# Kernel optimization log

Hardware: AMD Instinct MI355X
Metric: run time of the kernel (lower is better)

## Reference

```python
import jax, jax.numpy as jnp
import numpy as np

NUM_HEADS = 16
HEAD_DIM = 80  # head_dim_ori; NPU pads 80->128 with zeros (math-neutral)


def _rotate_half(x):
    x1, x2 = jnp.split(x, 2, axis=-1)
    return jnp.concatenate([-x2, x1], axis=-1)


def setup_inputs() -> dict:
    key = jax.random.key(0)
    ks = jax.random.split(key, 7)
    S, E = 4096, 1280
    inv = jnp.asarray(1.0 / np.sqrt(E), jnp.float32)
    # rotary tables: proper cos/sin from angles for realism
    pos = jnp.arange(S, dtype=jnp.float32)[:, None]
    freqs = 1.0 / (10000.0 ** (jnp.arange(0, HEAD_DIM // 2, dtype=jnp.float32) / (HEAD_DIM // 2)))
    ang = pos * freqs[None, :]                      # [S, 40]
    ang = jnp.concatenate([ang, ang], axis=-1)      # [S, 80] rotate-half layout
    return {
        'hidden_states': jax.random.normal(ks[0], (S, E), jnp.float32),
        'cos': jnp.cos(ang),
        'sin': jnp.sin(ang),
        'w_qkv': jax.random.normal(ks[1], (3 * E, E), jnp.float32) * inv,
        'b_qkv': jax.random.normal(ks[2], (3 * E,), jnp.float32) * 0.02,
        'w_proj': jax.random.normal(ks[3], (E, E), jnp.float32) * inv,
        'b_proj': jax.random.normal(ks[4], (E,), jnp.float32) * 0.02,
    }


def reference(hidden_states, cos, sin, w_qkv, b_qkv, w_proj, b_proj):
    S, E = hidden_states.shape
    H, D = NUM_HEADS, HEAD_DIM
    # fused QKV linear (transposeB=True, hasBias=True) then split into 3
    qkv = hidden_states @ w_qkv.T + b_qkv          # [S, 3E]
    q, k, v = jnp.split(qkv, 3, axis=-1)
    q = q.reshape(S, H, D)
    k = k.reshape(S, H, D)
    v = v.reshape(S, H, D)
    # rotate-half RoPE (rotaryCoeff=2) on q and k
    c = cos[:, None, :]
    s = sin[:, None, :]
    q = q * c + _rotate_half(q) * s
    k = k * c + _rotate_half(k) * s
    # full bidirectional self-attention (PA_ENCODER), qkScale = 1/sqrt(head_dim_ori)
    scale = jnp.asarray(1.0 / np.sqrt(D), q.dtype)
    scores = jnp.einsum('shd,thd->hst', q, k) * scale   # [H, S, S]
    attn = jax.nn.softmax(scores, axis=-1)
    out = jnp.einsum('hst,thd->shd', attn, v).reshape(S, E)
    # output projection + residual add (atten_res_add)
    dense = out @ w_proj.T + b_proj
    return hidden_states + dense
```

## Files before the change

kernel.cpp:

```cpp
#include <hip/hip_runtime.h>
#include <hip/hip_bf16.h>


#define S_LEN 4096
#define E_DIM 1280
#define NH 16
#define HD 80
#define HDP 96

typedef __bf16 bf16x8 __attribute__((ext_vector_type(8)));
typedef float f32x4 __attribute__((ext_vector_type(4)));

__device__ __forceinline__ short f2bf(float x) {
    __hip_bfloat16 h = __float2bfloat16(x);
    return __builtin_bit_cast(short, h);
}
__device__ __forceinline__ float bf2f(short x) {
    return __bfloat162float(__builtin_bit_cast(__hip_bfloat16, x));
}
__device__ __forceinline__ bf16x8 ldb(const short* p) {
    return *reinterpret_cast<const bf16x8*>(p);
}
__device__ __forceinline__ unsigned cvt_pk_bf16(float a, float b) {
    unsigned r;
    asm("v_cvt_pk_bf16_f32 %0, %1, %2" : "=v"(r) : "v"(a), "v"(b));
    return r;
}
__device__ __forceinline__ void gload16(const void* g, void* l) {
    __builtin_amdgcn_global_load_lds(
        (const __attribute__((address_space(1))) unsigned int*)g,
        (__attribute__((address_space(3))) unsigned int*)l, 16, 0, 0);
}

__global__ __launch_bounds__(256) void cast3_k(const float* __restrict__ a, short* __restrict__ oa, int na4,
                                               const float* __restrict__ b, short* __restrict__ ob, int nb4,
                                               const float* __restrict__ c, short* __restrict__ oc, int nc4,
                                               short* __restrict__ Qg, short* __restrict__ Kg, int nd4) {
    int j = blockIdx.x * 256 + threadIdx.x;
    const float* src;
    short* dst;
    bool remap = false;
    if (j < na4) {
        src = a; dst = oa;
    } else {
        j -= na4;
        if (j < nb4) {
            src = b; dst = ob; remap = true;
        } else {
            j -= nb4;
            if (j < nc4) {
                src = c; dst = oc;
            } else {
                j -= nc4;
                if (j >= nd4) return;
                int half = nd4 >> 1;
                short* base = (j < half) ? Qg : Kg;
                int rem = (j < half) ? j : j - half;
                int hs = rem >> 1, gp = rem & 1;
                int4 z = {0, 0, 0, 0};
                *reinterpret_cast<int4*>(&base[(size_t)hs * HDP + 80 + gp * 8]) = z;
                return;
            }
        }
    }
    float4 v = *reinterpret_cast<const float4*>(&src[j * 4]);
    int dj = j;
    if (remap) {
        int row = j / 320, c4 = j - row * 320;
        if (row < 2560) {
            int part = row / 1280;
            int loc = row - part * 1280;
            int hh = loc / 80, d = loc - hh * 80;
            int dp = (d < 40) ? 2 * d : 2 * (d - 40) + 1;
            dj = (part * 1280 + hh * 80 + dp) * 320 + c4;
        }
    }
    ushort4 o;
    o.x = (unsigned short)f2bf(v.x);
    o.y = (unsigned short)f2bf(v.y);
    o.z = (unsigned short)f2bf(v.z);
    o.w = (unsigned short)f2bf(v.w);
    *reinterpret_cast<ushort4*>(&dst[dj * 4]) = o;
}

__global__ __launch_bounds__(512, 2) void gemm1_256_k(
    const short* __restrict__ A, const short* __restrict__ B, const float* __restrict__ bias,
    const float* __restrict__ cosp, const float* __restrict__ sinp,
    short* __restrict__ Qg, short* __restrict__ Kg, short* __restrict__ Vt) {
    const int K = E_DIM;
    __shared__ __align__(16) short smem[65536];
#define AS_(d, kh) (smem + (d)*16384 + (kh)*8192)
#define BS_(d, kh) (smem + 32768 + (d)*16384 + (kh)*8192)
    int t = threadIdx.x;
    int lane = t & 63, w = t >> 6;
    int wr = w >> 2, wc = w & 3;
    int lr = lane & 15, lg = lane >> 4;
    int bid = blockIdx.x;
    int swz = (bid & 7) * 30 + (bid >> 3);
    int bm = swz / 15, bn = swz % 15;
    int mb = bm * 256, nb = bn * 256;

    int lgs = (t & 3) ^ ((t >> 3) & 3);
    const short* aS = A + (size_t)(mb + (t >> 2)) * K + lgs * 8;
    const short* bS = B + (size_t)(nb + (t >> 2)) * K + lgs * 8;
    const int rowStep = 128 * K;

    int aoff[2][4], boff[4];
#pragma unroll
    for (int mq = 0; mq < 2; mq++)
#pragma unroll
        for (int ii = 0; ii < 4; ii++) {
            int r = wr * 128 + mq * 64 + ii * 16 + lr;
            aoff[mq][ii] = r * 32 + ((lg ^ ((r >> 1) & 3)) * 8);
        }
#pragma unroll
    for (int n = 0; n < 4; n++) {
        int r = wc * 64 + n * 16 + lr;
        boff[n] = r * 32 + ((lg ^ ((r >> 1) & 3)) * 8);
    }

    f32x4 acc[8][4];
#pragma unroll
    for (int i = 0; i < 8; i++)
#pragma unroll
        for (int n = 0; n < 4; n++) acc[i][n] = (f32x4){0.f, 0.f, 0.f, 0.f};

#define STG_A(d, kh, kb2)                                              \
    {                                                                  \
        gload16(aS + (kb2) + (kh)*32, AS_(d, kh) + w * 512);           \
        gload16(aS + rowStep + (kb2) + (kh)*32, AS_(d, kh) + 4096 + w * 512); \
    }
#define STG_B(d, kh, kb2)                                              \
    {                                                                  \
        gload16(bS + (kb2) + (kh)*32, BS_(d, kh) + w * 512);           \
        gload16(bS + rowStep + (kb2) + (kh)*32, BS_(d, kh) + 4096 + w * 512); \
    }

    STG_A(0, 0, 0);
    STG_B(0, 0, 0);
    STG_A(0, 1, 0);
    STG_B(0, 1, 0);
    asm volatile("s_waitcnt vmcnt(4)" ::: "memory");
    __builtin_amdgcn_s_barrier();
    asm volatile("" ::: "memory");

    for (int kb = 0; kb < K; kb += 64) {
        int d = (kb >> 6) & 1;
        int kb2 = kb + 64;
        bool more = kb2 < K;
        bf16x8 af[4], bfr[4];

#pragma unroll
        for (int n = 0; n < 4; n++) bfr[n] = ldb(&BS_(d, 0)[boff[n]]);
#pragma unroll
        for (int ii = 0; ii < 4; ii++) af[ii] = ldb(&AS_(d, 0)[aoff[0][ii]]);
        if (more) STG_A(d ^ 1, 0, kb2);
        __builtin_amdgcn_s_barrier();
        asm volatile("s_waitcnt lgkmcnt(0)" ::: "memory");
        __builtin_amdgcn_sched_barrier(0);
        __builtin_amdgcn_s_setprio(1);
#pragma unroll
        for (int ii = 0; ii < 4; ii++)
#pragma unroll
            for (int n = 0; n < 4; n++)
                acc[ii][n] = __builtin_amdgcn_mfma_f32_16x16x32_bf16(af[ii], bfr[n], acc[ii][n], 0, 0, 0);
        __builtin_amdgcn_s_setprio(0);
        __builtin_amdgcn_s_barrier();
        asm volatile("" ::: "memory");

#pragma unroll
        for (int ii = 0; ii < 4; ii++) af[ii] = ldb(&AS_(d, 0)[aoff[1][ii]]);
        if (more) {
            STG_B(d ^ 1, 0, kb2);
            asm volatile("s_waitcnt vmcnt(4)" ::: "memory");
        } else {
            asm volatile("s_waitcnt vmcnt(0)" ::: "memory");
        }
        __builtin_amdgcn_s_barrier();
        asm volatile("s_waitcnt lgkmcnt(0)" ::: "memory");
        __builtin_amdgcn_sched_barrier(0);
        __builtin_amdgcn_s_setprio(1);
#pragma unroll
        for (int ii = 0; ii < 4; ii++)
#pragma unroll
            for (int n = 0; n < 4; n++)
                acc[4 + ii][n] = __builtin_amdgcn_mfma_f32_16x16x32_bf16(af[ii], bfr[n], acc[4 + ii][n], 0, 0, 0);
        __builtin_amdgcn_s_setprio(0);
        __builtin_amdgcn_s_barrier();
        asm volatile("" ::: "memory");

#pragma unroll
        for (int n = 0; n < 4; n++) bfr[n] = ldb(&BS_(d, 1)[boff[n]]);
#pragma unroll
        for (int ii = 0; ii < 4; ii++) af[ii] = ldb(&AS_(d, 1)[aoff[0][ii]]);
        if (more) STG_A(d ^ 1, 1, kb2);
        __builtin_amdgcn_s_barrier();
        asm volatile("s_waitcnt lgkmcnt(0)" ::: "memory");
        __builtin_amdgcn_sched_barrier(0);
        __builtin_amdgcn_s_setprio(1);
#pragma unroll
        for (int ii = 0; ii < 4; ii++)
#pragma unroll
            for (int n = 0; n < 4; n++)
                acc[ii][n] = __builtin_amdgcn_mfma_f32_16x16x32_bf16(af[ii], bfr[n], acc[ii][n], 0, 0, 0);
        __builtin_amdgcn_s_setprio(0);
        __builtin_amdgcn_s_barrier();
        asm volatile("" ::: "memory");

#pragma unroll
        for (int ii = 0; ii < 4; ii++) af[ii] = ldb(&AS_(d, 1)[aoff[1][ii]]);
        if (more) {
            STG_B(d ^ 1, 1, kb2);
            asm volatile("s_waitcnt vmcnt(4)" ::: "memory");
        }
        __builtin_amdgcn_s_barrier();
        asm volatile("s_waitcnt lgkmcnt(0)" ::: "memory");
        __builtin_amdgcn_sched_barrier(0);
        __builtin_amdgcn_s_setprio(1);
#pragma unroll
        for (int ii = 0; ii < 4; ii++)
#pragma unroll
            for (int n = 0; n < 4; n++)
                acc[4 + ii][n] = __builtin_amdgcn_mfma_f32_16x16x32_bf16(af[ii], bfr[n], acc[4 + ii][n], 0, 0, 0);
        __builtin_amdgcn_s_setprio(0);
        __builtin_amdgcn_s_barrier();
        asm volatile("" ::: "memory");
    }
#undef STG_A
#undef STG_B

    int part = nb / E_DIM;
    int nloc = nb - part * E_DIM;
    if (part < 2) {
#pragma unroll
        for (int j = 0; j < 4; j++) {
            int c = wc * 64 + j * 16 + lr;
            int pcol = nloc + c;
            int hh = pcol / 80, dl = pcol - hh * 80;
            float bv = bias[part * E_DIM + hh * 80 + ((dl & 1) ? (dl >> 1) + 40 : (dl >> 1))];
            int cw = c & 7, cg = c >> 3;
#pragma unroll
            for (int i = 0; i < 8; i++) {
#pragma unroll
                for (int r = 0; r < 4; r++) {
                    int s = wr * 128 + (i >> 2) * 64 + (i & 3) * 16 + lg * 4 + r;
                    smem[s * 256 + (((cg ^ ((s >> 2) & 3)) << 3) | cw)] = f2bf(acc[i][j][r] + bv);
                }
            }
        }
        __syncthreads();
        short* dst = part ? Kg : Qg;
        const float qs = part ? 1.0f : 0.16129849190f;
#pragma unroll
        for (int k = 0; k < 16; k++) {
            int g = t + k * 512;
            int row = g >> 5, gc = g & 31;
            int pg = gc ^ ((row >> 2) & 3);
            int4 v = *reinterpret_cast<const int4*>(&smem[row * 256 + pg * 8]);
            int s = mb + row;
            int pcol = nloc + gc * 8;
            int hh = pcol / 80;
            int dl = pcol - hh * 80;
            int i2 = dl >> 1;
            float4 cs = *reinterpret_cast<const float4*>(&cosp[s * HD + i2]);
            float4 sn = *reinterpret_cast<const float4*>(&sinp[s * HD + i2]);
            const short* sp = reinterpret_cast<const short*>(&v);
            float f[8];
#pragma unroll
            for (int i = 0; i < 8; i++) f[i] = bf2f(sp[i]);
            float c0 = cs.x * qs, s0 = sn.x * qs;
            float c1 = cs.y * qs, s1 = sn.y * qs;
            float c2 = cs.z * qs, s2 = sn.z * qs;
            float c3 = cs.w * qs, s3 = sn.w * qs;
            uint4 pw;
            pw.x = cvt_pk_bf16(f[0] * c0 - f[1] * s0, f[1] * c0 + f[0] * s0);
            pw.y = cvt_pk_bf16(f[2] * c1 - f[3] * s1, f[3] * c1 + f[2] * s1);
            pw.z = cvt_pk_bf16(f[4] * c2 - f[5] * s2, f[5] * c2 + f[4] * s2);
            pw.w = cvt_pk_bf16(f[6] * c3 - f[7] * s3, f[7] * c3 + f[6] * s3);
            *reinterpret_cast<uint4*>(&dst[((size_t)hh * S_LEN + s) * HDP + dl]) = pw;
        }
    } else {
#pragma unroll
        for (int j = 0; j < 4; j++) {
            int c = wc * 64 + j * 16 + lr;
            float bv = bias[nb + c];
            int cw = c & 7, cg = c >> 3;
#pragma unroll
            for (int i = 0; i < 8; i++) {
#pragma unroll
                for (int r = 0; r < 4; r++) {
                    int s = wr * 128 + (i >> 2) * 64 + (i & 3) * 16 + lg * 4 + r;
                    int vs = ((s >> 2) & 7) ^ ((s >> 5) & 7);
                    smem[s * 256 + (((cg ^ vs) << 3) | cw)] = f2bf(acc[i][j][r] + bv);
                }
            }
        }
        __syncthreads();
#pragma unroll
        for (int k = 0; k < 16; k++) {
            int g = t + k * 512;
            int lc = g >> 5;
            int sgrp = (g >> 2) & 7, oct = g & 3;
            int cg = lc >> 3, cw = lc & 7;
            short tmp[8];
#pragma unroll
            for (int q = 0; q < 8; q++) {
                int key = oct * 4 + (q & 3) + ((q >> 2) << 4);
                int sl = sgrp * 32 + key;
                int vs = (key >> 2) ^ sgrp;
                tmp[q] = smem[sl * 256 + (((cg ^ vs) << 3) | cw)];
            }
            int vcol = nloc + lc;
            int hh = vcol / 80, dl = vcol - hh * 80;
            *reinterpret_cast<int4*>(
                &Vt[(size_t)(hh * HD + dl) * S_LEN + mb + sgrp * 32 + oct * 8]) =
                *reinterpret_cast<int4*>(tmp);
        }
    }
#undef AS_
#undef BS_
}

__global__ __launch_bounds__(256) void gemm_bt_k(
    const short* __restrict__ A, const short* __restrict__ B, const float* __restrict__ bias,
    const float* __restrict__ resid, float* __restrict__ Out) {
    const int K = E_DIM;
    __shared__ short As[2][128 * 64];
    __shared__ short Bs[2][128 * 64];
    int t = threadIdx.x;
    int lane = t & 63, w = t >> 6;
    int wr = w >> 1, wc = w & 1;
    int lr = lane & 15, lg = lane >> 4;
    int mb = blockIdx.y * 128, nb = blockIdx.x * 128;

    const short* asrc[4];
    const short* bsrc[4];
#pragma unroll
    for (int c = 0; c < 4; c++) {
        int p = c * 256 + t;
        int m = p >> 3;
        int kg = (p & 7) ^ (m & 7);
        asrc[c] = A + (size_t)(mb + m) * K + kg * 8;
        bsrc[c] = B + (size_t)(nb + m) * K + kg * 8;
    }
    int xa = lr & 7;
    int cx0 = ((0 * 4 + lg) ^ xa) * 8;
    int cx1 = ((1 * 4 + lg) ^ xa) * 8;
    int rowA[4], rowB[4];
#pragma unroll
    for (int i = 0; i < 4; i++) {
        rowA[i] = (wr * 64 + i * 16 + lr) * 64;
        rowB[i] = (wc * 64 + i * 16 + lr) * 64;
    }

    f32x4 acc[4][4];
#pragma unroll
    for (int i = 0; i < 4; i++)
#pragma unroll
        for (int j = 0; j < 4; j++) acc[i][j] = (f32x4){0.f, 0.f, 0.f, 0.f};

#define G_STAGE(buf, kb)                                             \
    {                                                                \
        _Pragma("unroll") for (int c = 0; c < 4; c++) {              \
            int ldso = c * 2048 + w * 512;                           \
            gload16(asrc[c] + (kb), &As[buf][ldso]);                 \
            gload16(bsrc[c] + (kb), &Bs[buf][ldso]);                 \
        }                                                            \
    }

    G_STAGE(0, 0);
    asm volatile("s_waitcnt vmcnt(0)" ::: "memory");
    __syncthreads();

    int buf = 0;
    for (int kb = 0; kb < K; kb += 64) {
        if (kb + 64 < K) G_STAGE(buf ^ 1, kb + 64);
        __builtin_amdgcn_s_setprio(1);
#pragma unroll
        for (int kk = 0; kk < 2; kk++) {
            int cx = kk ? cx1 : cx0;
            bf16x8 af[4], bfr[4];
#pragma unroll
            for (int i = 0; i < 4; i++) {
                af[i] = ldb(&As[buf][rowA[i] + cx]);
                bfr[i] = ldb(&Bs[buf][rowB[i] + cx]);
            }
#pragma unroll
            for (int i = 0; i < 4; i++)
#pragma unroll
                for (int j = 0; j < 4; j++)
                    acc[i][j] = __builtin_amdgcn_mfma_f32_16x16x32_bf16(af[i], bfr[j], acc[i][j], 0, 0, 0);
        }
        __builtin_amdgcn_s_setprio(0);
        __syncthreads();
        buf ^= 1;
    }
#undef G_STAGE

#pragma unroll
    for (int j = 0; j < 4; j++) {
        int n = nb + wc * 64 + j * 16 + lr;
        float bv = bias[n];
#pragma unroll
        for (int i = 0; i < 4; i++) {
#pragma unroll
            for (int r = 0; r < 4; r++) {
                int s = mb + wr * 64 + i * 16 + lg * 4 + r;
                Out[s * E_DIM + n] = acc[i][j][r] + bv + resid[s * E_DIM + n];
            }
        }
    }
}

__global__ __launch_bounds__(512, 4) void attn_k(const short* __restrict__ Qg,
                                                 const short* __restrict__ Kg,
                                                 const short* __restrict__ Vt,
                                                 short* __restrict__ Ob) {
    __shared__ __align__(16) short smem[24832];
    short* ksb = smem;
    short* vsb = smem + 13312;

    int t = threadIdx.x;
    int lane = t & 63, w = t >> 6;
    int lr = lane & 15, lg = lane >> 4;
    int pairi = w >> 1, half = w & 1;
    int L = blockIdx.x;
    int h = ((L & 7) << 1) | (L >> 8);
    int qb = ((L >> 3) & 31) << 7;

    const short* kgp = Kg + (size_t)h * S_LEN * HDP;
    const short* vgp = Vt + (size_t)h * HD * S_LEN;

    bf16x8 qf[2][3];
#pragma unroll
    for (int qq = 0; qq < 2; qq++) {
        const short* qp = Qg + ((size_t)h * S_LEN + qb + pairi * 32 + qq * 16 + lr) * HDP;
#pragma unroll
        for (int kk = 0; kk < 3; kk++) qf[qq][kk] = ldb(qp + kk * 32 + lg * 8);
    }
    f32x4 o[2][5];
#pragma unroll
    for (int qq = 0; qq < 2; qq++)
#pragma unroll
        for (int nd = 0; nd < 5; nd++) o[qq][nd] = (f32x4){0.f, 0.f, 0.f, 0.f};
    f32x4 l4[2] = {(f32x4){0.f, 0.f, 0.f, 0.f}, (f32x4){0.f, 0.f, 0.f, 0.f}};

    int gk0 = t, rk0 = gk0 / 13, ok0 = gk0 % 13;
    if (ok0 == 12) ok0 = 0;
    const short* ksrc0 = kgp + rk0 * HDP + ok0 * 8;
    int gk1 = t + 512, rk1 = gk1 / 13, ok1 = gk1 % 13;
    if (ok1 == 12) ok1 = 0;
    const short* ksrc1 = kgp + rk1 * HDP + ok1 * 8;
    int gv0 = t, rv0 = gv0 / 9, ov0 = gv0 % 9;
    if (ov0 == 8) ov0 = 0;
    const short* vsrc0 = vgp + (size_t)rv0 * S_LEN + ov0 * 8;
    bool v1v = (t + 512) < 720;
    int gv1 = t + 512, rv1 = gv1 / 9, ov1 = gv1 % 9;
    if (ov1 == 8) ov1 = 0;
    const short* vsrc1 = vgp + (size_t)rv1 * S_LEN + ov1 * 8;

#define A_STAGE(buf, kb)                                                          \
    {                                                                             \
        gload16(ksrc0 + (size_t)(kb) * HDP, ksb + (buf)*6656 + w * 512);          \
        if (w < 5) gload16(ksrc1 + (size_t)(kb) * HDP, ksb + (buf)*6656 + 4096 + w * 512); \
        gload16(vsrc0 + (kb), vsb + (buf)*5760 + w * 512);                        \
        if (v1v) gload16(vsrc1 + (kb), vsb + (buf)*5760 + 4096 + w * 512);        \
    }

    A_STAGE(0, 0);
    asm volatile("s_waitcnt vmcnt(0)" ::: "memory");
    __syncthreads();

    int buf = 0;
    for (int kb = 0; kb < S_LEN; kb += 64) {
        if (kb + 64 < S_LEN) A_STAGE(buf ^ 1, kb + 64);
        const short* ks = ksb + buf * 6656;
        const short* vs = vsb + buf * 5760;

        f32x4 sc[2][2];
#pragma unroll
        for (int qq = 0; qq < 2; qq++)
#pragma unroll
            for (int n = 0; n < 2; n++) sc[qq][n] = (f32x4){0.f, 0.f, 0.f, 0.f};
        __builtin_amdgcn_s_setprio(1);
#pragma unroll
        for (int n = 0; n < 2; n++) {
#pragma unroll
            for (int kk = 0; kk < 3; kk++) {
                bf16x8 kf = ldb(&ks[(half * 32 + n * 16 + lr) * 104 + kk * 32 + lg * 8]);
                sc[0][n] = __builtin_amdgcn_mfma_f32_16x16x32_bf16(kf, qf[0][kk], sc[0][n], 0, 0, 0);
                sc[1][n] = __builtin_amdgcn_mfma_f32_16x16x32_bf16(kf, qf[1][kk], sc[1][n], 0, 0, 0);
            }
        }
        __builtin_amdgcn_s_setprio(0);

        bf16x8 pa[2];
#pragma unroll
        for (int qq = 0; qq < 2; qq++) {
#pragma unroll
            for (int n = 0; n < 2; n++) {
#pragma unroll
                for (int r = 0; r < 4; r++) sc[qq][n][r] = __builtin_amdgcn_exp2f(sc[qq][n][r]);
                l4[qq] += sc[qq][n];
            }
            uint4 pw;
            pw.x = cvt_pk_bf16(sc[qq][0][0], sc[qq][0][1]);
            pw.y = cvt_pk_bf16(sc[qq][0][2], sc[qq][0][3]);
            pw.z = cvt_pk_bf16(sc[qq][1][0], sc[qq][1][1]);
            pw.w = cvt_pk_bf16(sc[qq][1][2], sc[qq][1][3]);
            pa[qq] = __builtin_bit_cast(bf16x8, pw);
        }

        __builtin_amdgcn_s_setprio(1);
#pragma unroll
        for (int nd = 0; nd < 5; nd++) {
            bf16x8 vf = ldb(&vs[(nd * 16 + lr) * 72 + half * 32 + lg * 8]);
            o[0][nd] = __builtin_amdgcn_mfma_f32_16x16x32_bf16(pa[0], vf, o[0][nd], 0, 0, 0);
            o[1][nd] = __builtin_amdgcn_mfma_f32_16x16x32_bf16(pa[1], vf, o[1][nd], 0, 0, 0);
        }
        __builtin_amdgcn_s_setprio(0);

        __syncthreads();
        buf ^= 1;
    }
#undef A_STAGE

    float lh[2];
#pragma unroll
    for (int qq = 0; qq < 2; qq++) {
        float l = l4[qq][0] + l4[qq][1] + l4[qq][2] + l4[qq][3];
        l += __shfl_xor(l, 16);
        l += __shfl_xor(l, 32);
        lh[qq] = l;
    }
    float* Osc = reinterpret_cast<float*>(smem);
    float* lsc = reinterpret_cast<float*>(smem) + 10240;
    if (half) {
#pragma unroll
        for (int qq = 0; qq < 2; qq++) {
#pragma unroll
            for (int nd = 0; nd < 5; nd++)
#pragma unroll
                for (int r = 0; r < 4; r++)
                    Osc[(pairi * 32 + qq * 16 + lg * 4 + r) * 80 + nd * 16 + lr] = o[qq][nd][r];
            if (lg == 0) lsc[pairi * 32 + qq * 16 + lr] = lh[qq];
        }
    }
    __syncthreads();
    if (!half) {
        float rl[2][4];
#pragma unroll
        for (int qq = 0; qq < 2; qq++) {
            float lt = lh[qq] + lsc[pairi * 32 + qq * 16 + lr];
#pragma unroll
            for (int r = 0; r < 4; r++) {
                float lf = __shfl(lt, lg * 4 + r);
                rl[qq][r] = __builtin_amdgcn_rcpf(lf);
            }
        }
#pragma unroll
        for (int qq = 0; qq < 2; qq++)
#pragma unroll
            for (int nd = 0; nd < 5; nd++)
#pragma unroll
                for (int r = 0; r < 4; r++) {
                    int s = qb + pairi * 32 + qq * 16 + lg * 4 + r;
                    float val = o[qq][nd][r] + Osc[(pairi * 32 + qq * 16 + lg * 4 + r) * 80 + nd * 16 + lr];
                    Ob[s * E_DIM + h * HD + nd * 16 + lr] = f2bf(val * rl[qq][r]);
                }
    }
}

extern "C" void kernel_launch(void* const* d_in, const int* in_sizes, int n_in,
                              void* d_out, int out_size, void* d_ws, size_t ws_size,
                              hipStream_t stream) {
    const float* hidden = (const float*)d_in[0];
    const float* cosp = (const float*)d_in[1];
    const float* sinp = (const float*)d_in[2];
    const float* wqkv = (const float*)d_in[3];
    const float* bqkv = (const float*)d_in[4];
    const float* wproj = (const float*)d_in[5];
    const float* bproj = (const float*)d_in[6];
    float* out = (float*)d_out;

    char* p = (char*)d_ws;
    short* Xb = (short*)p;      p += (size_t)S_LEN * E_DIM * 2;
    short* Wqkvb = (short*)p;   p += (size_t)3 * E_DIM * E_DIM * 2;
    short* Wprojb = (short*)p;  p += (size_t)E_DIM * E_DIM * 2;
    short* Qg = (short*)p;      p += (size_t)NH * S_LEN * HDP * 2;
    short* Kg = (short*)p;      p += (size_t)NH * S_LEN * HDP * 2;
    short* Vt = (short*)p;      p += (size_t)NH * HD * S_LEN * 2;
    short* Ob = Xb;

    const int na4 = S_LEN * E_DIM / 4;
    const int nb4 = 3 * E_DIM * E_DIM / 4;
    const int nc4 = E_DIM * E_DIM / 4;
    const int nd4 = 2 * NH * S_LEN * 2;
    cast3_k<<<(na4 + nb4 + nc4 + nd4 + 255) / 256, 256, 0, stream>>>(
        hidden, Xb, na4, wqkv, Wqkvb, nb4, wproj, Wprojb, nc4, Qg, Kg, nd4);

    gemm1_256_k<<<dim3(240), 512, 0, stream>>>(Xb, Wqkvb, bqkv, cosp, sinp, Qg, Kg, Vt);

    attn_k<<<dim3(512), 512, 0, stream>>>(Qg, Kg, Vt, Ob);

    gemm_bt_k<<<dim3(E_DIM / 128, S_LEN / 128), 256, 0, stream>>>(
        Ob, Wprojb, bproj, hidden, out);
}
```

Baseline: 178.6 us.

## Halve attention block threads, give each wave 64 query rows

The attention kernel now launches 256 threads per block (4 waves, 2 pairs) instead of 512, and each wave handles 4 query sub-tiles of 16 rows instead of 2. The 128-row query tile per block is unchanged. Each K/V fragment read from shared memory now feeds twice as many MFMAs, which cuts LDS traffic and barrier cost per FLOP. In exchange, register pressure roughly doubles for the accumulators and Q fragments, launch bounds drop to 2 blocks per CU, and the global-to-LDS staging is redistributed across fewer threads.

```diff
diff --git a/kernel.cpp b/kernel.cpp
--- a/kernel.cpp
+++ b/kernel.cpp
@@ -412,7 +412,7 @@
     }
 }
 
-__global__ __launch_bounds__(512, 4) void attn_k(const short* __restrict__ Qg,
+__global__ __launch_bounds__(256, 2) void attn_k(const short* __restrict__ Qg,
                                                  const short* __restrict__ Kg,
                                                  const short* __restrict__ Vt,
                                                  short* __restrict__ Ob) {
@@ -431,40 +431,50 @@
     const short* kgp = Kg + (size_t)h * S_LEN * HDP;
     const short* vgp = Vt + (size_t)h * HD * S_LEN;
 
-    bf16x8 qf[2][3];
-#pragma unroll
-    for (int qq = 0; qq < 2; qq++) {
-        const short* qp = Qg + ((size_t)h * S_LEN + qb + pairi * 32 + qq * 16 + lr) * HDP;
+    bf16x8 qf[4][3];
+#pragma unroll
+    for (int qq = 0; qq < 4; qq++) {
+        const short* qp = Qg + ((size_t)h * S_LEN + qb + pairi * 64 + qq * 16 + lr) * HDP;
 #pragma unroll
         for (int kk = 0; kk < 3; kk++) qf[qq][kk] = ldb(qp + kk * 32 + lg * 8);
     }
-    f32x4 o[2][5];
-#pragma unroll
-    for (int qq = 0; qq < 2; qq++)
+    f32x4 o[4][5];
+#pragma unroll
+    for (int qq = 0; qq < 4; qq++)
 #pragma unroll
         for (int nd = 0; nd < 5; nd++) o[qq][nd] = (f32x4){0.f, 0.f, 0.f, 0.f};
-    f32x4 l4[2] = {(f32x4){0.f, 0.f, 0.f, 0.f}, (f32x4){0.f, 0.f, 0.f, 0.f}};
-
-    int gk0 = t, rk0 = gk0 / 13, ok0 = gk0 % 13;
-    if (ok0 == 12) ok0 = 0;
-    const short* ksrc0 = kgp + rk0 * HDP + ok0 * 8;
-    int gk1 = t + 512, rk1 = gk1 / 13, ok1 = gk1 % 13;
-    if (ok1 == 12) ok1 = 0;
-    const short* ksrc1 = kgp + rk1 * HDP + ok1 * 8;
-    int gv0 = t, rv0 = gv0 / 9, ov0 = gv0 % 9;
-    if (ov0 == 8) ov0 = 0;
-    const short* vsrc0 = vgp + (size_t)rv0 * S_LEN + ov0 * 8;
-    bool v1v = (t + 512) < 720;
-    int gv1 = t + 512, rv1 = gv1 / 9, ov1 = gv1 % 9;
-    if (ov1 == 8) ov1 = 0;
-    const short* vsrc1 = vgp + (size_t)rv1 * S_LEN + ov1 * 8;
-
-#define A_STAGE(buf, kb)                                                          \
-    {                                                                             \
-        gload16(ksrc0 + (size_t)(kb) * HDP, ksb + (buf)*6656 + w * 512);          \
-        if (w < 5) gload16(ksrc1 + (size_t)(kb) * HDP, ksb + (buf)*6656 + 4096 + w * 512); \
-        gload16(vsrc0 + (kb), vsb + (buf)*5760 + w * 512);                        \
-        if (v1v) gload16(vsrc1 + (kb), vsb + (buf)*5760 + 4096 + w * 512);        \
+    f32x4 l4[4];
+#pragma unroll
+    for (int qq = 0; qq < 4; qq++) l4[qq] = (f32x4){0.f, 0.f, 0.f, 0.f};
+
+    const short* ksrc[4];
+#pragma unroll
+    for (int i = 0; i < 4; i++) {
+        int g = t + i * 256;
+        int rk = g / 13, ok = g % 13;
+        if (ok == 12) ok = 0;
+        if (g < 832) ksrc[i] = kgp + rk * HDP + ok * 8;
+        else ksrc[i] = kgp;
+    }
+    const short* vsrc[3];
+#pragma unroll
+    for (int i = 0; i < 3; i++) {
+        int g = t + i * 256;
+        int rv = g / 9, ov = g % 9;
+        if (ov == 8) ov = 0;
+        if (g < 720) vsrc[i] = vgp + (size_t)rv * S_LEN + ov * 8;
+        else vsrc[i] = vgp;
+    }
+
+#define A_STAGE(buf, kb)                                                           \
+    {                                                                              \
+        gload16(ksrc[0] + (size_t)(kb) * HDP, ksb + (buf)*6656 + w * 512);         \
+        gload16(ksrc[1] + (size_t)(kb) * HDP, ksb + (buf)*6656 + 2048 + w * 512);  \
+        gload16(ksrc[2] + (size_t)(kb) * HDP, ksb + (buf)*6656 + 4096 + w * 512);  \
+        if (t < 64) gload16(ksrc[3] + (size_t)(kb) * HDP, ksb + (buf)*6656 + 6144 + w * 512); \
+        gload16(vsrc[0] + (kb), vsb + (buf)*5760 + w * 512);                       \
+        gload16(vsrc[1] + (kb), vsb + (buf)*5760 + 2048 + w * 512);                \
+        if (t < 208) gload16(vsrc[2] + (kb), vsb + (buf)*5760 + 4096 + w * 512);   \
     }
 
     A_STAGE(0, 0);
@@ -477,9 +487,9 @@
         const short* ks = ksb + buf * 6656;
         const short* vs = vsb + buf * 5760;
 
-        f32x4 sc[2][2];
-#pragma unroll
-        for (int qq = 0; qq < 2; qq++)
+        f32x4 sc[4][2];
+#pragma unroll
+        for (int qq = 0; qq < 4; qq++)
 #pragma unroll
             for (int n = 0; n < 2; n++) sc[qq][n] = (f32x4){0.f, 0.f, 0.f, 0.f};
         __builtin_amdgcn_s_setprio(1);
@@ -490,13 +500,15 @@
                 bf16x8 kf = ldb(&ks[(half * 32 + n * 16 + lr) * 104 + kk * 32 + lg * 8]);
                 sc[0][n] = __builtin_amdgcn_mfma_f32_16x16x32_bf16(kf, qf[0][kk], sc[0][n], 0, 0, 0);
                 sc[1][n] = __builtin_amdgcn_mfma_f32_16x16x32_bf16(kf, qf[1][kk], sc[1][n], 0, 0, 0);
+                sc[2][n] = __builtin_amdgcn_mfma_f32_16x16x32_bf16(kf, qf[2][kk], sc[2][n], 0, 0, 0);
+                sc[3][n] = __builtin_amdgcn_mfma_f32_16x16x32_bf16(kf, qf[3][kk], sc[3][n], 0, 0, 0);
             }
         }
         __builtin_amdgcn_s_setprio(0);
 
-        bf16x8 pa[2];
-#pragma unroll
-        for (int qq = 0; qq < 2; qq++) {
+        bf16x8 pa[4];
+#pragma unroll
+        for (int qq = 0; qq < 4; qq++) {
 #pragma unroll
             for (int n = 0; n < 2; n++) {
 #pragma unroll
@@ -517,6 +529,8 @@
             bf16x8 vf = ldb(&vs[(nd * 16 + lr) * 72 + half * 32 + lg * 8]);
             o[0][nd] = __builtin_amdgcn_mfma_f32_16x16x32_bf16(pa[0], vf, o[0][nd], 0, 0, 0);
             o[1][nd] = __builtin_amdgcn_mfma_f32_16x16x32_bf16(pa[1], vf, o[1][nd], 0, 0, 0);
+            o[2][nd] = __builtin_amdgcn_mfma_f32_16x16x32_bf16(pa[2], vf, o[2][nd], 0, 0, 0);
+            o[3][nd] = __builtin_amdgcn_mfma_f32_16x16x32_bf16(pa[3], vf, o[3][nd], 0, 0, 0);
         }
         __builtin_amdgcn_s_setprio(0);
 
@@ -525,9 +539,9 @@
     }
 #undef A_STAGE
 
-    float lh[2];
-#pragma unroll
-    for (int qq = 0; qq < 2; qq++) {
+    float lh[4];
+#pragma unroll
+    for (int qq = 0; qq < 4; qq++) {
         float l = l4[qq][0] + l4[qq][1] + l4[qq][2] + l4[qq][3];
         l += __shfl_xor(l, 16);
         l += __shfl_xor(l, 32);
@@ -537,21 +551,21 @@
     float* lsc = reinterpret_cast<float*>(smem) + 10240;
     if (half) {
 #pragma unroll
-        for (int qq = 0; qq < 2; qq++) {
+        for (int qq = 0; qq < 4; qq++) {
 #pragma unroll
             for (int nd = 0; nd < 5; nd++)
 #pragma unroll
                 for (int r = 0; r < 4; r++)
-                    Osc[(pairi * 32 + qq * 16 + lg * 4 + r) * 80 + nd * 16 + lr] = o[qq][nd][r];
-            if (lg == 0) lsc[pairi * 32 + qq * 16 + lr] = lh[qq];
+                    Osc[(pairi * 64 + qq * 16 + lg * 4 + r) * 80 + nd * 16 + lr] = o[qq][nd][r];
+            if (lg == 0) lsc[pairi * 64 + qq * 16 + lr] = lh[qq];
         }
     }
     __syncthreads();
     if (!half) {
-        float rl[2][4];
-#pragma unroll
-        for (int qq = 0; qq < 2; qq++) {
-            float lt = lh[qq] + lsc[pairi * 32 + qq * 16 + lr];
+        float rl[4][4];
+#pragma unroll
+        for (int qq = 0; qq < 4; qq++) {
+            float lt = lh[qq] + lsc[pairi * 64 + qq * 16 + lr];
 #pragma unroll
             for (int r = 0; r < 4; r++) {
                 float lf = __shfl(lt, lg * 4 + r);
@@ -559,13 +573,13 @@
             }
         }
 #pragma unroll
-        for (int qq = 0; qq < 2; qq++)
+        for (int qq = 0; qq < 4; qq++)
 #pragma unroll
             for (int nd = 0; nd < 5; nd++)
 #pragma unroll
                 for (int r = 0; r < 4; r++) {
-                    int s = qb + pairi * 32 + qq * 16 + lg * 4 + r;
-                    float val = o[qq][nd][r] + Osc[(pairi * 32 + qq * 16 + lg * 4 + r) * 80 + nd * 16 + lr];
+                    int s = qb + pairi * 64 + qq * 16 + lg * 4 + r;
+                    float val = o[qq][nd][r] + Osc[(pairi * 64 + qq * 16 + lg * 4 + r) * 80 + nd * 16 + lr];
                     Ob[s * E_DIM + h * HD + nd * 16 + lr] = f2bf(val * rl[qq][r]);
                 }
     }
@@ -601,7 +615,7 @@
 
     gemm1_256_k<<<dim3(240), 512, 0, stream>>>(Xb, Wqkvb, bqkv, cosp, sinp, Qg, Kg, Vt);
 
-    attn_k<<<dim3(512), 512, 0, stream>>>(Qg, Kg, Vt, Ob);
+    attn_k<<<dim3(512), 256, 0, stream>>>(Qg, Kg, Vt, Ob);
 
     gemm_bt_k<<<dim3(E_DIM / 128, S_LEN / 128), 256, 0, stream>>>(
         Ob, Wprojb, bproj, hidden, out);
```

After: 181.1 us. No clear change (+1.4%).
